# Performance work log

Hardware: AMD Instinct MI355X
Metric: run time of the kernel (lower is better)

## Reference

```python
import jax, jax.numpy as jnp
import numpy as np

N = 50000      # nodes
E = 800000     # edges
D = 128        # h_dim
R = 8          # num_rel
B = 4          # num_bases (< R -> basis decomposition)
L = 2          # num_conv
BN_EPS = 1e-3  # keras BatchNormalization default epsilon


def setup_inputs() -> dict:
    key = jax.random.key(0)
    ks = jax.random.split(key, 10)
    node_feat = jax.random.normal(ks[0], (N, D), dtype=jnp.float32)
    src = jax.random.randint(ks[1], (E,), 0, N)
    dst = jax.random.randint(ks[2], (E,), 0, N)
    etype = jax.random.randint(ks[3], (E,), 0, R)
    s = 1.0 / np.sqrt(D)
    W_emb = jax.random.normal(ks[4], (D, D), dtype=jnp.float32) * s
    b_emb = jnp.zeros((D,), dtype=jnp.float32)
    bases = jax.random.normal(ks[5], (L, B, D, D), dtype=jnp.float32) * s
    w_coe = jax.random.normal(ks[6], (L, R, B), dtype=jnp.float32) * 0.3
    self_loop = jax.random.normal(ks[7], (L, D, D), dtype=jnp.float32) * s
    bn_gamma = jnp.ones((L, D), dtype=jnp.float32)
    bn_beta = jnp.zeros((L, D), dtype=jnp.float32)
    bn_mean = jnp.zeros((L, D), dtype=jnp.float32)
    bn_var = jnp.ones((L, D), dtype=jnp.float32)
    return {"node_feat": node_feat, "W_emb": W_emb, "b_emb": b_emb,
            "bases": bases, "w_coe": w_coe, "self_loop": self_loop,
            "bn_gamma": bn_gamma, "bn_beta": bn_beta,
            "bn_mean": bn_mean, "bn_var": bn_var,
            "src": src, "dst": dst, "etype": etype}


def _edge_norm(etype, dst, dtype):
    # compute_norm: per edge type r, node_norm[dst] = 1/(#edges of type r into dst),
    # later types overwrite earlier ones (tensor_scatter_nd_update in the loop).
    node_norm = jnp.zeros((N,), dtype=dtype)
    for r in range(R):  # unique edge types, fixed ascending order
        mask = (etype == r).astype(dtype)
        cnt = jax.ops.segment_sum(mask, dst, num_segments=N)
        node_norm = jnp.where(cnt > 0, 1.0 / jnp.maximum(cnt, 1.0), node_norm)
    return node_norm[dst][:, None]  # [E, 1], norm of each edge's destination


def reference(node_feat, W_emb, b_emb, bases, w_coe, self_loop,
              bn_gamma, bn_beta, bn_mean, bn_var, src, dst, etype):
    # embedding Dense
    h = node_feat @ W_emb + b_emb                     # [N, D]
    norm = _edge_norm(etype, dst, h.dtype)            # [E, 1]
    for l in range(L):
        # basis decomposition: W[r] = sum_b w_coe[r,b] * bases[b]
        W = jnp.einsum('rb,bdf->rdf', w_coe[l], bases[l])   # [R, D, D]
        # transform all nodes under every relation, then gather per edge
        # (same math as per-type boolean_mask + matmul in low_mem path)
        T = jnp.einsum('nd,rdf->rnf', h, W)                 # [R, N, D]
        msg = T[etype, src] * norm                          # [E, D]
        agg = jax.ops.segment_sum(msg, dst, num_segments=N) # sum reduce -> [N, D]
        h = agg + h @ self_loop[l]
        # BatchNormalization, inference mode (training=None)
        h = bn_gamma[l] * (h - bn_mean[l]) * jax.lax.rsqrt(bn_var[l] + BN_EPS) + bn_beta[l]
        h = jax.nn.relu(h)
        # Dropout is identity at inference
    return h
```

## Files before the change

### kernel.cpp

```cpp
#include <hip/hip_runtime.h>

#define Dh 128
#define NN 50000
#define EE 800000
#define RR 8
#define BB 4
#define LL 2
#define KTOT 640
#define KA0 512
#define BN_EPS 1e-3f
#define NR (NN * RR)
#define NBLK 196

#define N8    (NN * Dh / 8)
#define BT_N  (LL * Dh * KTOT)
#define WE_N  (Dh * Dh)
#define EPI_N (3 * Dh)
#define Z4_N  (NR / 4)
#define PREP_TOT (N8 + BT_N + WE_N + EPI_N + Z4_N)

typedef __attribute__((ext_vector_type(8))) short bf16x8;
typedef __attribute__((ext_vector_type(4))) float f32x4;
typedef __attribute__((ext_vector_type(2))) float f32x2;

__device__ inline unsigned short f2bf(float x) {
    unsigned u = __float_as_uint(x);
    unsigned r = (u + 0x7fffu + ((u >> 16) & 1u)) >> 16;
    return (unsigned short)r;
}

__global__ __launch_bounds__(256) void prep_kernel(
    const float* __restrict__ nf, const float* __restrict__ bases,
    const float* __restrict__ self_loop, const float* __restrict__ W_emb,
    const float* __restrict__ b_emb,
    const float* __restrict__ bn_gamma, const float* __restrict__ bn_beta,
    const float* __restrict__ bn_mean, const float* __restrict__ bn_var,
    unsigned short* __restrict__ nf_bf, unsigned short* __restrict__ BT,
    unsigned short* __restrict__ WembT,
    float* __restrict__ sc, float* __restrict__ sh, int* __restrict__ counts)
{
    int idx = blockIdx.x * 256 + threadIdx.x;
    if (idx < N8) {
        size_t base = (size_t)idx * 8;
        float4 v0 = *(const float4*)&nf[base];
        float4 v1 = *(const float4*)&nf[base + 4];
        unsigned short o[8] = { f2bf(v0.x), f2bf(v0.y), f2bf(v0.z), f2bf(v0.w),
                                f2bf(v1.x), f2bf(v1.y), f2bf(v1.z), f2bf(v1.w) };
        *(uint4*)&nf_bf[base] = *(uint4*)o;
        return;
    }
    idx -= N8;
    if (idx < BT_N) {
        int l = idx / (Dh * KTOT);
        int rem = idx - l * (Dh * KTOT);
        int f = rem / KTOT;
        int k = rem - f * KTOT;
        float v;
        if (k < KA0) v = bases[(((l * BB + (k >> 7)) * Dh) + (k & 127)) * Dh + f];
        else         v = self_loop[((size_t)l * Dh + (k - KA0)) * Dh + f];
        BT[(size_t)(l * Dh + f) * KTOT + k] = f2bf(v);
        return;
    }
    idx -= BT_N;
    if (idx < WE_N) {
        int f = idx >> 7, d = idx & 127;
        WembT[f * Dh + d] = f2bf(W_emb[d * Dh + f]);
        return;
    }
    idx -= WE_N;
    if (idx < EPI_N) {
        int cfg = idx >> 7, d = idx & 127;
        float s, t;
        if (cfg == 0) { s = 1.f; t = b_emb[d]; }
        else {
            int l = cfg - 1;
            float sv = bn_gamma[l * Dh + d] * rsqrtf(bn_var[l * Dh + d] + BN_EPS);
            s = sv;
            t = bn_beta[l * Dh + d] - bn_mean[l * Dh + d] * sv;
        }
        sc[cfg * Dh + d] = s; sh[cfg * Dh + d] = t;
        return;
    }
    idx -= EPI_N;
    if (idx < Z4_N) ((int4*)counts)[idx] = make_int4(0, 0, 0, 0);
}

__global__ __launch_bounds__(256) void gemm_bn_kernel(
    const unsigned short* __restrict__ A0, int ka0,
    const unsigned short* __restrict__ A1,
    const unsigned short* __restrict__ BT, int K,
    const float* __restrict__ sc, const float* __restrict__ sh,
    void* __restrict__ outp, int out_fp32, int do_relu, int M)
{
    __shared__ unsigned short a_s[64][72];
    __shared__ unsigned short b_s[128][72];
    int t = threadIdx.x;
    int wave = t >> 6, lane = t & 63;
    int n16 = lane & 15, quad = lane >> 4;
    int row0 = blockIdx.x * 64;

    f32x4 acc[8];
    #pragma unroll
    for (int j = 0; j < 8; j++) acc[j] = (f32x4){0.f, 0.f, 0.f, 0.f};

    int nchunk = K >> 6;
    for (int ch = 0; ch < nchunk; ch++) {
        int k0 = ch * 64;
        {
            int srow = t >> 2, seg = t & 3;
            int gr = row0 + srow;
            int kk = k0 + seg * 16;
            const uint4* gp;
            if (kk < ka0) gp = (const uint4*)&A0[(size_t)gr * ka0 + kk];
            else          gp = (const uint4*)&A1[(size_t)gr * Dh + (kk - ka0)];
            #pragma unroll
            for (int i = 0; i < 2; i++) {
                uint4 v = make_uint4(0u, 0u, 0u, 0u);
                if (gr < M) v = gp[i];
                *(uint4*)&a_s[srow][seg * 16 + i * 8] = v;
            }
        }
        {
            int f = t >> 1, seg = t & 1;
            const uint4* bp = (const uint4*)&BT[(size_t)f * K + k0 + seg * 32];
            #pragma unroll
            for (int i = 0; i < 4; i++)
                *(uint4*)&b_s[f][seg * 32 + i * 8] = bp[i];
        }
        __syncthreads();
        #pragma unroll
        for (int ks = 0; ks < 2; ks++) {
            bf16x8 af, bfr[8];
            af = *(const bf16x8*)&a_s[wave * 16 + n16][ks * 32 + quad * 8];
            #pragma unroll
            for (int j = 0; j < 8; j++)
                bfr[j] = *(const bf16x8*)&b_s[j * 16 + n16][ks * 32 + quad * 8];
            #pragma unroll
            for (int j = 0; j < 8; j++)
                acc[j] = __builtin_amdgcn_mfma_f32_16x16x32_bf16(
                    af, bfr[j], acc[j], 0, 0, 0);
        }
        __syncthreads();
    }

    float sj[8], tj[8];
    #pragma unroll
    for (int j = 0; j < 8; j++) {
        int col = j * 16 + n16;
        sj[j] = sc[col]; tj[j] = sh[col];
    }
    #pragma unroll
    for (int v = 0; v < 4; v++) {
        int gr = row0 + wave * 16 + quad * 4 + v;
        if (gr < M) {
            #pragma unroll
            for (int j = 0; j < 8; j++) {
                float y = acc[j][v] * sj[j] + tj[j];
                if (do_relu) y = fmaxf(y, 0.f);
                int col = j * 16 + n16;
                if (out_fp32) ((float*)outp)[(size_t)gr * Dh + col] = y;
                else ((unsigned short*)outp)[(size_t)gr * Dh + col] = f2bf(y);
            }
        }
    }
}

__global__ __launch_bounds__(256) void count_kernel(
    const int* __restrict__ dst, const int* __restrict__ etype,
    int* __restrict__ counts, unsigned short* __restrict__ rank)
{
    int idx = blockIdx.x * 256 + threadIdx.x;
    if (idx >= EE / 4) return;
    int4 d = ((const int4*)dst)[idx];
    int4 t = ((const int4*)etype)[idx];
    int r0 = atomicAdd(&counts[d.x * RR + t.x], 1);
    int r1 = atomicAdd(&counts[d.y * RR + t.y], 1);
    int r2 = atomicAdd(&counts[d.z * RR + t.z], 1);
    int r3 = atomicAdd(&counts[d.w * RR + t.w], 1);
    ((ushort4*)rank)[idx] = make_ushort4((unsigned short)r0, (unsigned short)r1,
                                         (unsigned short)r2, (unsigned short)r3);
}

__global__ __launch_bounds__(256) void norm_scan1_kernel(
    int* __restrict__ counts, float* __restrict__ node_norm,
    int* __restrict__ row_ptr, int* __restrict__ bsum)
{
    __shared__ int s[256];
    int t = threadIdx.x;
    int n = blockIdx.x * 256 + t;
    int total = 0; float norm = 0.f;
    if (n < NN) {
        int pre[RR];
        #pragma unroll
        for (int r = 0; r < RR; r++) {
            int c = counts[n * RR + r];
            pre[r] = total;
            total += c;
            if (c > 0) norm = 1.0f / (float)c;
        }
        #pragma unroll
        for (int r = 0; r < RR; r++) counts[n * RR + r] = pre[r];
        node_norm[n] = norm;
    }
    s[t] = total;
    __syncthreads();
    #pragma unroll
    for (int off = 1; off < 256; off <<= 1) {
        int v = (t >= off) ? s[t - off] : 0;
        __syncthreads();
        s[t] += v;
        __syncthreads();
    }
    if (n < NN) row_ptr[n] = s[t] - total;
    if (t == 255) bsum[blockIdx.x] = s[255];
}

__global__ __launch_bounds__(256) void scan2_kernel(
    const int* __restrict__ bsum, int* __restrict__ boffset)
{
    __shared__ int s[256];
    int t = threadIdx.x;
    int d = (t < NBLK) ? bsum[t] : 0;
    s[t] = d;
    __syncthreads();
    #pragma unroll
    for (int off = 1; off < 256; off <<= 1) {
        int v = (t >= off) ? s[t - off] : 0;
        __syncthreads();
        s[t] += v;
        __syncthreads();
    }
    if (t <= NBLK) boffset[t] = s[t] - d;
}

__global__ __launch_bounds__(256) void scan3_kernel(
    int* __restrict__ row_ptr, int* __restrict__ counts,
    const int* __restrict__ boffset)
{
    int t = threadIdx.x;
    int n = blockIdx.x * 256 + t;
    if (n < NN) {
        int v = row_ptr[n] + boffset[blockIdx.x];
        row_ptr[n] = v;
        #pragma unroll
        for (int r = 0; r < RR; r++) counts[n * RR + r] += v;
    }
    if (blockIdx.x == 0 && t == 0) row_ptr[NN] = EE;
}

__global__ __launch_bounds__(256) void fill_kernel(
    const int* __restrict__ src, const int* __restrict__ dst,
    const int* __restrict__ etype, const unsigned short* __restrict__ rank,
    const int* __restrict__ counts, unsigned* __restrict__ packed)
{
    int idx = blockIdx.x * 256 + threadIdx.x;
    if (idx >= EE / 4) return;
    int4 d  = ((const int4*)dst)[idx];
    int4 sr = ((const int4*)src)[idx];
    int4 et = ((const int4*)etype)[idx];
    ushort4 rk = ((const ushort4*)rank)[idx];
    int p0 = counts[d.x * RR + et.x] + rk.x;
    int p1 = counts[d.y * RR + et.y] + rk.y;
    int p2 = counts[d.z * RR + et.z] + rk.z;
    int p3 = counts[d.w * RR + et.w] + rk.w;
    packed[p0] = (unsigned)sr.x | ((unsigned)et.x << 16);
    packed[p1] = (unsigned)sr.y | ((unsigned)et.y << 16);
    packed[p2] = (unsigned)sr.z | ((unsigned)et.z << 16);
    packed[p3] = (unsigned)sr.w | ((unsigned)et.w << 16);
}

__global__ __launch_bounds__(256) void agg_basis_kernel(
    const unsigned* __restrict__ h32, const int* __restrict__ row_ptr,
    const unsigned* __restrict__ packed, const float* __restrict__ node_norm,
    const float* __restrict__ wco,
    unsigned* __restrict__ aggB)
{
    __shared__ float4 co_s[RR];
    int t = threadIdx.x;
    if (t < RR) co_s[t] = ((const float4*)wco)[t];
    __syncthreads();
    int wave = t >> 6, lane = t & 63;
    int n = blockIdx.x * 4 + wave;
    if (n >= NN) return;
    int s = row_ptr[n];
    int e = row_ptr[n + 1];
    f32x2 a[BB];
    #pragma unroll
    for (int b = 0; b < BB; b++) a[b] = (f32x2){0.f, 0.f};
    int i = s;
    for (; i + 8 <= e; i += 8) {
        unsigned p[8], hv[8];
        #pragma unroll
        for (int k = 0; k < 8; k++) p[k] = packed[i + k];
        #pragma unroll
        for (int k = 0; k < 8; k++)
            hv[k] = h32[(size_t)(p[k] & 0xffffu) * 64 + lane];
        #pragma unroll
        for (int k = 0; k < 8; k++) {
            float4 co = co_s[p[k] >> 16];
            f32x2 v = (f32x2){ __uint_as_float(hv[k] << 16),
                               __uint_as_float(hv[k] & 0xffff0000u) };
            a[0] += co.x * v;
            a[1] += co.y * v;
            a[2] += co.z * v;
            a[3] += co.w * v;
        }
    }
    if (i < e) {
        unsigned p[8], hv[8];
        #pragma unroll
        for (int k = 0; k < 8; k++) {
            int j = i + k;
            p[k] = packed[j < e ? j : (e - 1)];
        }
        #pragma unroll
        for (int k = 0; k < 8; k++)
            hv[k] = h32[(size_t)(p[k] & 0xffffu) * 64 + lane];
        #pragma unroll
        for (int k = 0; k < 8; k++) {
            float vm = (i + k < e) ? 1.f : 0.f;
            float4 co = co_s[p[k] >> 16];
            f32x2 v = (f32x2){ __uint_as_float(hv[k] << 16) * vm,
                               __uint_as_float(hv[k] & 0xffff0000u) * vm };
            a[0] += co.x * v;
            a[1] += co.y * v;
            a[2] += co.z * v;
            a[3] += co.w * v;
        }
    }
    float norm = node_norm[n];
    #pragma unroll
    for (int b = 0; b < BB; b++) {
        unsigned o = (unsigned)f2bf(a[b].x * norm) |
                     ((unsigned)f2bf(a[b].y * norm) << 16);
        aggB[(size_t)n * 256 + b * 64 + lane] = o;
    }
}

extern "C" void kernel_launch(void* const* d_in, const int* in_sizes, int n_in,
                              void* d_out, int out_size, void* d_ws, size_t ws_size,
                              hipStream_t stream)
{
    const float* node_feat = (const float*)d_in[0];
    const float* W_emb     = (const float*)d_in[1];
    const float* b_emb     = (const float*)d_in[2];
    const float* bases     = (const float*)d_in[3];
    const float* w_coe     = (const float*)d_in[4];
    const float* self_loop = (const float*)d_in[5];
    const float* bn_gamma  = (const float*)d_in[6];
    const float* bn_beta   = (const float*)d_in[7];
    const float* bn_mean   = (const float*)d_in[8];
    const float* bn_var    = (const float*)d_in[9];
    const int*   src       = (const int*)d_in[10];
    const int*   dst       = (const int*)d_in[11];
    const int*   etype     = (const int*)d_in[12];

    char* ws = (char*)d_ws;
    size_t off = 0;
    unsigned short* h0 = (unsigned short*)(ws + off);     off += (size_t)NN * Dh * 2;
    unsigned short* h1 = (unsigned short*)(ws + off);     off += (size_t)NN * Dh * 2;
    unsigned short* nf_bf = (unsigned short*)(ws + off);  off += (size_t)NN * Dh * 2;
    unsigned short* aggB = (unsigned short*)(ws + off);   off += (size_t)NN * KA0 * 2;
    unsigned short* BT = (unsigned short*)(ws + off);     off += (size_t)LL * Dh * KTOT * 2;
    unsigned short* WembT = (unsigned short*)(ws + off);  off += (size_t)Dh * Dh * 2;
    float* sc = (float*)(ws + off);                       off += 3 * Dh * 4;
    float* sh = (float*)(ws + off);                       off += 3 * Dh * 4;
    float* node_norm = (float*)(ws + off);                off += (size_t)NN * 4;
    int* counts = (int*)(ws + off);                       off += (size_t)NR * 4;
    int* row_ptr = (int*)(ws + off);                      off += ((size_t)NN + 4) * 4;
    unsigned short* rank = (unsigned short*)(ws + off);   off += (size_t)EE * 2;
    int* bsum = (int*)(ws + off);                         off += 256 * 4;
    int* boffset = (int*)(ws + off);                      off += 260 * 4;
    unsigned* packed = (unsigned*)(ws + off);             off += (size_t)EE * 4;

    const int e4_blocks = (EE / 4 + 255) / 256;
    const int node_blocks = (NN + 255) / 256;
    const int prep_blocks = (PREP_TOT + 255) / 256;
    const int gemm_blocks = (NN + 63) / 64;
    const int agg_blocks = (NN + 3) / 4;

    prep_kernel<<<prep_blocks, 256, 0, stream>>>(
        node_feat, bases, self_loop, W_emb, b_emb,
        bn_gamma, bn_beta, bn_mean, bn_var,
        nf_bf, BT, WembT, sc, sh, counts);

    count_kernel<<<e4_blocks, 256, 0, stream>>>(dst, etype, counts, rank);
    norm_scan1_kernel<<<node_blocks, 256, 0, stream>>>(counts, node_norm, row_ptr, bsum);
    scan2_kernel<<<1, 256, 0, stream>>>(bsum, boffset);
    scan3_kernel<<<node_blocks, 256, 0, stream>>>(row_ptr, counts, boffset);
    fill_kernel<<<e4_blocks, 256, 0, stream>>>(src, dst, etype, rank, counts, packed);

    gemm_bn_kernel<<<gemm_blocks, 256, 0, stream>>>(
        nf_bf, Dh, nullptr, WembT, Dh, sc, sh, h0, 0, 0, NN);

    agg_basis_kernel<<<agg_blocks, 256, 0, stream>>>(
        (const unsigned*)h0, row_ptr, packed, node_norm, w_coe, (unsigned*)aggB);
    gemm_bn_kernel<<<gemm_blocks, 256, 0, stream>>>(
        aggB, KA0, h0, BT, KTOT, sc + Dh, sh + Dh, h1, 0, 1, NN);

    agg_basis_kernel<<<agg_blocks, 256, 0, stream>>>(
        (const unsigned*)h1, row_ptr, packed, node_norm, w_coe + RR * BB, (unsigned*)aggB);
    gemm_bn_kernel<<<gemm_blocks, 256, 0, stream>>>(
        aggB, KA0, h1, BT + Dh * KTOT, KTOT, sc + 2 * Dh, sh + 2 * Dh, d_out, 1, 1, NN);
}
```

Measured before the change: 293.5 us.

## Split each wave into two half-waves gathering different edges with 8-byte loads

After: 347.0 us. +18.2%, slower.

```diff
diff --git a/kernel.cpp b/kernel.cpp
--- a/kernel.cpp
+++ b/kernel.cpp
@@ -27,6 +27,10 @@
     unsigned u = __float_as_uint(x);
     unsigned r = (u + 0x7fffu + ((u >> 16) & 1u)) >> 16;
     return (unsigned short)r;
+}
+
+__device__ inline unsigned packbf2(float x, float y) {
+    return (unsigned)f2bf(x) | ((unsigned)f2bf(y) << 16);
 }
 
 __global__ __launch_bounds__(256) void prep_kernel(
@@ -284,56 +288,94 @@
     if (n >= NN) return;
     int s = row_ptr[n];
     int e = row_ptr[n + 1];
-    f32x2 a[BB];
-    #pragma unroll
-    for (int b = 0; b < BB; b++) a[b] = (f32x2){0.f, 0.f};
+    int half = lane >> 5;
+    int hl = lane & 31;
+
+    f32x2 a[BB][2];
+    #pragma unroll
+    for (int b = 0; b < BB; b++) {
+        a[b][0] = (f32x2){0.f, 0.f};
+        a[b][1] = (f32x2){0.f, 0.f};
+    }
+
     int i = s;
+    if ((i & 1) && i < e) {
+        unsigned p = packed[i];
+        uint2 hv = *(const uint2*)&h32[(size_t)(p & 0xffffu) * 64 + hl * 2];
+        float4 co = co_s[p >> 16];
+        float vm = (half == 0) ? 1.f : 0.f;
+        f32x2 v0 = (f32x2){ __uint_as_float(hv.x << 16) * vm,
+                            __uint_as_float(hv.x & 0xffff0000u) * vm };
+        f32x2 v1 = (f32x2){ __uint_as_float(hv.y << 16) * vm,
+                            __uint_as_float(hv.y & 0xffff0000u) * vm };
+        a[0][0] += co.x * v0; a[0][1] += co.x * v1;
+        a[1][0] += co.y * v0; a[1][1] += co.y * v1;
+        a[2][0] += co.z * v0; a[2][1] += co.z * v1;
+        a[3][0] += co.w * v0; a[3][1] += co.w * v1;
+        i++;
+    }
     for (; i + 8 <= e; i += 8) {
-        unsigned p[8], hv[8];
-        #pragma unroll
-        for (int k = 0; k < 8; k++) p[k] = packed[i + k];
-        #pragma unroll
-        for (int k = 0; k < 8; k++)
-            hv[k] = h32[(size_t)(p[k] & 0xffffu) * 64 + lane];
-        #pragma unroll
-        for (int k = 0; k < 8; k++) {
+        uint2 pp[4]; unsigned p[4]; uint2 hv[4];
+        #pragma unroll
+        for (int k = 0; k < 4; k++) pp[k] = *(const uint2*)&packed[i + 2 * k];
+        #pragma unroll
+        for (int k = 0; k < 4; k++) p[k] = half ? pp[k].y : pp[k].x;
+        #pragma unroll
+        for (int k = 0; k < 4; k++)
+            hv[k] = *(const uint2*)&h32[(size_t)(p[k] & 0xffffu) * 64 + hl * 2];
+        #pragma unroll
+        for (int k = 0; k < 4; k++) {
             float4 co = co_s[p[k] >> 16];
-            f32x2 v = (f32x2){ __uint_as_float(hv[k] << 16),
-                               __uint_as_float(hv[k] & 0xffff0000u) };
-            a[0] += co.x * v;
-            a[1] += co.y * v;
-            a[2] += co.z * v;
-            a[3] += co.w * v;
+            f32x2 v0 = (f32x2){ __uint_as_float(hv[k].x << 16),
+                                __uint_as_float(hv[k].x & 0xffff0000u) };
+            f32x2 v1 = (f32x2){ __uint_as_float(hv[k].y << 16),
+                                __uint_as_float(hv[k].y & 0xffff0000u) };
+            a[0][0] += co.x * v0; a[0][1] += co.x * v1;
+            a[1][0] += co.y * v0; a[1][1] += co.y * v1;
+            a[2][0] += co.z * v0; a[2][1] += co.z * v1;
+            a[3][0] += co.w * v0; a[3][1] += co.w * v1;
         }
     }
     if (i < e) {
-        unsigned p[8], hv[8];
-        #pragma unroll
-        for (int k = 0; k < 8; k++) {
-            int j = i + k;
-            p[k] = packed[j < e ? j : (e - 1)];
-        }
-        #pragma unroll
-        for (int k = 0; k < 8; k++)
-            hv[k] = h32[(size_t)(p[k] & 0xffffu) * 64 + lane];
-        #pragma unroll
-        for (int k = 0; k < 8; k++) {
-            float vm = (i + k < e) ? 1.f : 0.f;
-            float4 co = co_s[p[k] >> 16];
-            f32x2 v = (f32x2){ __uint_as_float(hv[k] << 16) * vm,
-                               __uint_as_float(hv[k] & 0xffff0000u) * vm };
-            a[0] += co.x * v;
-            a[1] += co.y * v;
-            a[2] += co.z * v;
-            a[3] += co.w * v;
-        }
+        uint2 pp[4]; unsigned p[4]; uint2 hv[4];
+        #pragma unroll
+        for (int k = 0; k < 4; k++) pp[k] = *(const uint2*)&packed[i + 2 * k];
+        #pragma unroll
+        for (int k = 0; k < 4; k++) p[k] = half ? pp[k].y : pp[k].x;
+        #pragma unroll
+        for (int k = 0; k < 4; k++)
+            hv[k] = *(const uint2*)&h32[(size_t)(p[k] & 0xffffu) * 64 + hl * 2];
+        #pragma unroll
+        for (int k = 0; k < 4; k++) {
+            int idx = i + 2 * k + half;
+            float vm = (idx < e) ? 1.f : 0.f;
+            float4 co = co_s[(p[k] >> 16) & 7u];
+            f32x2 v0 = (f32x2){ __uint_as_float(hv[k].x << 16) * vm,
+                                __uint_as_float(hv[k].x & 0xffff0000u) * vm };
+            f32x2 v1 = (f32x2){ __uint_as_float(hv[k].y << 16) * vm,
+                                __uint_as_float(hv[k].y & 0xffff0000u) * vm };
+            a[0][0] += co.x * v0; a[0][1] += co.x * v1;
+            a[1][0] += co.y * v0; a[1][1] += co.y * v1;
+            a[2][0] += co.z * v0; a[2][1] += co.z * v1;
+            a[3][0] += co.w * v0; a[3][1] += co.w * v1;
+        }
+    }
+    #pragma unroll
+    for (int b = 0; b < BB; b++) {
+        a[b][0].x += __shfl_xor(a[b][0].x, 32);
+        a[b][0].y += __shfl_xor(a[b][0].y, 32);
+        a[b][1].x += __shfl_xor(a[b][1].x, 32);
+        a[b][1].y += __shfl_xor(a[b][1].y, 32);
     }
     float norm = node_norm[n];
-    #pragma unroll
-    for (int b = 0; b < BB; b++) {
-        unsigned o = (unsigned)f2bf(a[b].x * norm) |
-                     ((unsigned)f2bf(a[b].y * norm) << 16);
-        aggB[(size_t)n * 256 + b * 64 + lane] = o;
+    int b0 = half ? 2 : 0;
+    #pragma unroll
+    for (int bb = 0; bb < 2; bb++) {
+        int b = b0 + bb;
+        uint2 o;
+        o.x = packbf2(a[b][0].x * norm, a[b][0].y * norm);
+        o.y = packbf2(a[b][1].x * norm, a[b][1].y * norm);
+        *(uint2*)&aggB[(size_t)n * 256 + b * 64 + hl * 2] = o;
     }
 }
 
@@ -371,7 +413,7 @@
     unsigned short* rank = (unsigned short*)(ws + off);   off += (size_t)EE * 2;
     int* bsum = (int*)(ws + off);                         off += 256 * 4;
     int* boffset = (int*)(ws + off);                      off += 260 * 4;
-    unsigned* packed = (unsigned*)(ws + off);             off += (size_t)EE * 4;
+    unsigned* packed = (unsigned*)(ws + off);             off += (size_t)EE * 4 + 64;
 
     const int e4_blocks = (EE / 4 + 255) / 256;
     const int node_blocks = (NN + 255) / 256;
```
